# Kernel tuning notes

Hardware: AMD Instinct MI355X
Metric: run time of the kernel (lower is better)

The kernel has to match this reference:

```python
import jax, jax.numpy as jnp
import numpy as np

T_NUM = 1024      # tracks
DET_NUM = 1024    # detections
DEG = 64          # candidate detections per track
E = T_NUM * DEG   # directed track->det edges (row<col half)
N = T_NUM + DET_NUM
D_IN = 512
D_EMB = 256
LAM = 5.0
SLACK = -0.2
SINKHORN_ITERS = 8


def setup_inputs() -> dict:
    key = jax.random.key(0)
    ks = jax.random.split(key, 20)
    x = jax.random.normal(ks[0], (N, D_IN), jnp.float32)
    coords = jax.random.uniform(ks[1], (N, 4), dtype=jnp.float32)
    r = jax.random.uniform(ks[2], (N, 4), dtype=jnp.float32)
    bx1 = r[:, 0] * 100.0; by1 = r[:, 1] * 100.0
    bw = r[:, 2] * 50.0 + 1.0; bh = r[:, 3] * 50.0 + 1.0
    coords_original = jnp.stack([bx1, by1, bx1 + bw, by1 + bh], axis=1)
    src_t = jnp.repeat(jnp.arange(T_NUM, dtype=jnp.int32), DEG)
    off = jnp.tile(jnp.arange(DEG, dtype=jnp.int32), T_NUM)
    dst_d = (src_t * 13 + off) % DET_NUM            # unique det per (track, slot)
    src = src_t
    dst = dst_d + T_NUM                              # detection node ids come after tracks
    edge_index = jnp.concatenate([jnp.stack([src, dst]), jnp.stack([dst, src])], axis=1)
    ground_truth = jax.random.bernoulli(ks[3], 0.1, (T_NUM * DET_NUM,)).astype(jnp.float32)

    def lin(k, i, o):
        return jax.random.normal(k, (i, o), jnp.float32) / np.sqrt(i).astype(np.float32)

    params = {
        'W_enc': lin(ks[4], D_IN, D_EMB), 'b_enc': jnp.zeros((D_EMB,), jnp.float32),
        'W1a': lin(ks[5], 2 * D_EMB, 64), 'b1a': jnp.zeros((64,), jnp.float32),
        'W2a': lin(ks[6], 64, 1), 'b2a': jnp.zeros((1,), jnp.float32),
        'W1g': lin(ks[7], 8, 16), 'b1g': jnp.zeros((16,), jnp.float32),
        'W2g': lin(ks[8], 16, 1), 'b2g': jnp.zeros((1,), jnp.float32),
        'W1f': lin(ks[9], 2, 8), 'b1f': jnp.zeros((8,), jnp.float32),
        'W2f': lin(ks[10], 8, 1), 'b2f': jnp.zeros((1,), jnp.float32),
        'Wn': lin(ks[11], D_EMB, D_EMB), 'Wm': lin(ks[12], D_EMB, D_EMB),
        'bo': jnp.zeros((D_EMB,), jnp.float32),
        'W1c': lin(ks[13], 2, 8), 'b1c': jnp.zeros((8,), jnp.float32),
        'W2c': lin(ks[14], 8, 1), 'b2c': jnp.zeros((1,), jnp.float32),
    }
    out = {'x': x, 'coords': coords, 'coords_original': coords_original,
           'ground_truth': ground_truth, 'edge_index': edge_index}
    out.update(params)
    return out


def _box_iou(a, b):
    # a, b: [E, 4] boxes (x1, y1, x2, y2)
    lt = jnp.maximum(a[:, :2], b[:, :2])
    rb = jnp.minimum(a[:, 2:], b[:, 2:])
    wh = jnp.clip(rb - lt, 0.0)
    inter = wh[:, 0] * wh[:, 1]
    area_a = (a[:, 2] - a[:, 0]) * (a[:, 3] - a[:, 1])
    area_b = (b[:, 2] - b[:, 0]) * (b[:, 3] - b[:, 1])
    return inter / (area_a + area_b - inter + 1e-9)


def _sinkhorn(M):
    def body(M, _):
        M = M / (jnp.sum(M, axis=1, keepdims=True) + 1e-9)
        M = M / (jnp.sum(M, axis=0, keepdims=True) + 1e-9)
        return M, None
    M, _ = jax.lax.scan(body, M, None, length=SINKHORN_ITERS)
    return M


def _forward(x, coords, coords_original,
             W_enc, b_enc, W1a, b1a, W2a, b2a, W1g, b1g, W2g, b2g,
             W1f, b1f, W2f, b2f, Wn, Wm, bo, W1c, b1c, W2c, b2c,
             edge_index):
    node = jax.nn.relu(x @ W_enc + b_enc)                      # [N, D_EMB]
    src, dst = edge_index[0], edge_index[1]                    # [2E]
    # batched per-edge appearance affinity (replaces python edge loop)
    pair = jnp.concatenate([node[src], node[dst]], axis=1)     # [2E, 2*D_EMB]
    a1 = jax.nn.relu(pair @ W1a + b1a) @ W2a + b2a             # [2E, 1]
    geo = jnp.concatenate([coords[src], coords[dst]], axis=1)  # [2E, 8]
    a2 = jax.nn.relu(geo @ W1g + b1g) @ W2g + b2g              # [2E, 1]
    e_in = jnp.concatenate([a1, a2], axis=1)                   # [2E, 2]
    edge_emb = jax.nn.relu(e_in @ W1f + b1f) @ W2f + b2f       # [2E, 1]
    # optim_net: one round of edge-weighted message passing
    msg = jax.ops.segment_sum(edge_emb * node[src], dst, num_segments=N)
    out = jax.nn.relu(node @ Wn + msg @ Wm + bo)               # [N, D_EMB]
    # forward (row < col) edges are the first E entries by construction
    sf, df = src[:E], dst[:E]
    oa, ob = out[sf], out[df]
    denom = jnp.maximum(jnp.linalg.norm(oa, axis=1) * jnp.linalg.norm(ob, axis=1), 1e-6)
    cosv = jnp.sum(oa * ob, axis=1) / denom                    # CosineSimilarity(dim=0) per edge
    iou = _box_iou(coords_original[sf], coords_original[df])   # [E]
    f_in = jnp.stack([cosv, iou], axis=1)                      # [E, 2]
    aff = (jax.nn.relu(f_in @ W1c + b1c) @ W2c + b2c)[:, 0]    # [E]
    # assignment matrix with slack row/col, scatter exp(aff*lam)
    slack_val = jnp.exp(jnp.float32(SLACK * LAM))
    M = jnp.full((T_NUM + 1, DET_NUM + 1), slack_val, jnp.float32)
    M = M.at[:T_NUM, :DET_NUM].set(0.0)
    M = M.at[sf, df - T_NUM].set(jnp.exp(aff * LAM))
    M = _sinkhorn(M)
    return M[:-1, :-1].reshape(-1)                             # [T_NUM*DET_NUM]


def reference(x, coords, coords_original, ground_truth, edge_index,
              W_enc, b_enc, W1a, b1a, W2a, b2a, W1g, b1g, W2g, b2g,
              W1f, b1f, W2f, b2f, Wn, Wm, bo, W1c, b1c, W2c, b2c):
    normalized_output = _forward(x, coords, coords_original,
                                 W_enc, b_enc, W1a, b1a, W2a, b2a,
                                 W1g, b1g, W2g, b2g, W1f, b1f, W2f, b2f,
                                 Wn, Wm, bo, W1c, b1c, W2c, b2c, edge_index)
    det_num = jnp.asarray(DET_NUM, jnp.int32)
    tracklet_num = jnp.asarray(T_NUM, jnp.int32)
    return (normalized_output, ground_truth, det_num, tracklet_num)
```

## Files before the change

kernel.cpp:

```cpp
#include <hip/hip_runtime.h>

#define T_NUM 1024
#define DET_NUM 1024
#define E_NUM 65536
#define TWO_E 131072
#define N_NODES 2048
#define D_IN 512
#define D_EMB 256

__device__ __forceinline__ unsigned bf16r(float x) {
  const unsigned u = __float_as_uint(x);
  return (u + 0x7fffu + ((u >> 16) & 1u)) >> 16;
}
__device__ __forceinline__ float bflo(unsigned p) { return __uint_as_float(p << 16); }
__device__ __forceinline__ float bfhi(unsigned p) { return __uint_as_float(p & 0xffff0000u); }
__device__ __forceinline__ void fma4(float4& a, float s, const float4 w) {
  a.x = fmaf(s, w.x, a.x); a.y = fmaf(s, w.y, a.y);
  a.z = fmaf(s, w.z, a.z); a.w = fmaf(s, w.w, a.w);
}

__global__ __launch_bounds__(512) void k_enc_pg(
    const float* __restrict__ x, const float* __restrict__ W,
    const float* __restrict__ b, const float* __restrict__ coords,
    const float* __restrict__ W1a, const float* __restrict__ W1g,
    float* __restrict__ node, float* __restrict__ P1, float* __restrict__ P2,
    float* __restrict__ G1, float* __restrict__ G2) {
  __shared__ __align__(16) float xsh[4][D_IN];
  __shared__ __align__(16) float pg[8][4][D_EMB];
  __shared__ __align__(16) float ns[4][D_EMB];
  __shared__ float pp1[4][64], pp2[4][64];
  const int tid = threadIdx.x;
  const int row0 = blockIdx.x * 4;
  {
    const int idx = tid * 4;
    const int r = idx >> 9, c = idx & 511;
    *reinterpret_cast<float4*>(&xsh[r][c]) =
        *reinterpret_cast<const float4*>(x + (size_t)(row0 + r) * D_IN + c);
  }
  __syncthreads();
  {
    const int kq = __builtin_amdgcn_readfirstlane(tid >> 6);
    const int jq = tid & 63;
    const float4* W4 = (const float4*)W;
    float4 a0 = make_float4(0.f, 0.f, 0.f, 0.f);
    float4 a1 = a0, a2 = a0, a3 = a0;
    const int kbeg = kq * 64;
    for (int k = kbeg; k < kbeg + 64; ++k) {
      const float4 w4 = W4[k * 64 + jq];
      fma4(a0, xsh[0][k], w4);
      fma4(a1, xsh[1][k], w4);
      fma4(a2, xsh[2][k], w4);
      fma4(a3, xsh[3][k], w4);
    }
    *reinterpret_cast<float4*>(&pg[kq][0][4 * jq]) = a0;
    *reinterpret_cast<float4*>(&pg[kq][1][4 * jq]) = a1;
    *reinterpret_cast<float4*>(&pg[kq][2][4 * jq]) = a2;
    *reinterpret_cast<float4*>(&pg[kq][3][4 * jq]) = a3;
  }
  __syncthreads();
  {
    const int r = tid >> 7, jc = tid & 127;
    float v0 = b[2 * jc + 0], v1 = b[2 * jc + 1];
#pragma unroll
    for (int kq = 0; kq < 8; kq++) {
      v0 += pg[kq][r][2 * jc + 0];
      v1 += pg[kq][r][2 * jc + 1];
    }
    v0 = fmaxf(v0, 0.f); v1 = fmaxf(v1, 0.f);
    *reinterpret_cast<float2*>(node + (size_t)(row0 + r) * D_EMB + 2 * jc) =
        make_float2(v0, v1);
    ns[r][2 * jc] = v0; ns[r][2 * jc + 1] = v1;
  }
  __syncthreads();
  const int r2 = tid >> 7, q2 = (tid >> 6) & 1, hh = tid & 63;
  float a1 = 0.f, a2 = 0.f;
  {
    const int k0 = q2 * 128;
    for (int k = 0; k < 128; k += 4) {
      const float4 nv = *reinterpret_cast<const float4*>(&ns[r2][k0 + k]);
      a1 = fmaf(nv.x, W1a[(k0 + k + 0) * 64 + hh], a1);
      a1 = fmaf(nv.y, W1a[(k0 + k + 1) * 64 + hh], a1);
      a1 = fmaf(nv.z, W1a[(k0 + k + 2) * 64 + hh], a1);
      a1 = fmaf(nv.w, W1a[(k0 + k + 3) * 64 + hh], a1);
      a2 = fmaf(nv.x, W1a[(D_EMB + k0 + k + 0) * 64 + hh], a2);
      a2 = fmaf(nv.y, W1a[(D_EMB + k0 + k + 1) * 64 + hh], a2);
      a2 = fmaf(nv.z, W1a[(D_EMB + k0 + k + 2) * 64 + hh], a2);
      a2 = fmaf(nv.w, W1a[(D_EMB + k0 + k + 3) * 64 + hh], a2);
    }
    if (q2 == 1) { pp1[r2][hh] = a1; pp2[r2][hh] = a2; }
  }
  __syncthreads();
  if (q2 == 0) {
    P1[(size_t)(row0 + r2) * 64 + hh] = a1 + pp1[r2][hh];
    P2[(size_t)(row0 + r2) * 64 + hh] = a2 + pp2[r2][hh];
  }
  if (tid < 64) {
    const int r = tid >> 4, g = tid & 15;
    const int n = row0 + r;
    float g1 = 0.f, g2 = 0.f;
#pragma unroll
    for (int k = 0; k < 4; k++) {
      const float c = coords[(size_t)n * 4 + k];
      g1 = fmaf(c, W1g[k * 16 + g], g1);
      g2 = fmaf(c, W1g[(4 + k) * 16 + g], g2);
    }
    G1[(size_t)n * 16 + g] = g1;
    G2[(size_t)n * 16 + g] = g2;
  }
}

__global__ __launch_bounds__(512) void k_msg_out(
    const float* __restrict__ node,
    const float* __restrict__ P1, const float* __restrict__ P2,
    const float* __restrict__ G1, const float* __restrict__ G2,
    const float* __restrict__ b1a, const float* __restrict__ W2a, const float* __restrict__ b2a,
    const float* __restrict__ b1g, const float* __restrict__ W2g, const float* __restrict__ b2g,
    const float* __restrict__ W1f, const float* __restrict__ b1f,
    const float* __restrict__ W2f, const float* __restrict__ b2f,
    const float* __restrict__ Wn, const float* __restrict__ Wm,
    const float* __restrict__ bo, float* __restrict__ outE, float* __restrict__ nrm) {
  __shared__ __align__(16) float msp[2][4][D_EMB];
  __shared__ __align__(16) float ms[4][D_EMB];
  __shared__ __align__(16) float nsh[4][D_EMB];
  __shared__ __align__(16) float pg[8][4][D_EMB];
  __shared__ float wsh[4][64];
  __shared__ int ssh[4][64];
  __shared__ float pa1[4][64], pa2[4][64];
  __shared__ float redn[8];
  const int tid = threadIdx.x;
  const int h = __builtin_amdgcn_readfirstlane(tid >> 8);
  const int j = tid & 255;
  const int row0 = blockIdx.x * 4;
  {
    const int r = (tid >> 6) & 3, o = tid & 63;
    const int n = row0 + r;
    int src;
    if (n < T_NUM) {
      src = T_NUM + ((13 * n + o) & 1023);
    } else {
      const int d = n - T_NUM;
      src = (709 * (d - o)) & 1023;
    }
    float a1p = 0.f, a2p = 0.f;
    const float4* p1 = (const float4*)(P1 + (size_t)src * 64) + h * 8;
    const float4* p2 = (const float4*)(P2 + (size_t)n * 64) + h * 8;
    const float4* b1 = (const float4*)b1a + h * 8;
    const float4* w2 = (const float4*)W2a + h * 8;
#pragma unroll
    for (int i = 0; i < 8; i++) {
      const float4 pa = p1[i], pb = p2[i], bb = b1[i], ww = w2[i];
      a1p += fmaxf(pa.x + pb.x + bb.x, 0.f) * ww.x + fmaxf(pa.y + pb.y + bb.y, 0.f) * ww.y +
             fmaxf(pa.z + pb.z + bb.z, 0.f) * ww.z + fmaxf(pa.w + pb.w + bb.w, 0.f) * ww.w;
    }
    const float4* g1 = (const float4*)(G1 + (size_t)src * 16) + h * 2;
    const float4* g2 = (const float4*)(G2 + (size_t)n * 16) + h * 2;
    const float4* bg = (const float4*)b1g + h * 2;
    const float4* wg = (const float4*)W2g + h * 2;
#pragma unroll
    for (int i = 0; i < 2; i++) {
      const float4 pa = g1[i], pb = g2[i], bb = bg[i], ww = wg[i];
      a2p += fmaxf(pa.x + pb.x + bb.x, 0.f) * ww.x + fmaxf(pa.y + pb.y + bb.y, 0.f) * ww.y +
             fmaxf(pa.z + pb.z + bb.z, 0.f) * ww.z + fmaxf(pa.w + pb.w + bb.w, 0.f) * ww.w;
    }
    if (h == 1) { pa1[r][o] = a1p; pa2[r][o] = a2p; ssh[r][o] = src; }
    else        { wsh[r][o] = a1p; pg[0][r][o] = a2p; }
  }
  __syncthreads();
  if (h == 0) {
    const int r = (tid >> 6) & 3, o = tid & 63;
    const float a1 = wsh[r][o] + pa1[r][o] + b2a[0];
    const float a2 = pg[0][r][o] + pa2[r][o] + b2g[0];
    float acc = b2f[0];
#pragma unroll
    for (int jj = 0; jj < 8; jj++) {
      const float hv = fmaxf(a1 * W1f[jj] + a2 * W1f[8 + jj] + b1f[jj], 0.f);
      acc = fmaf(hv, W2f[jj], acc);
    }
    wsh[r][o] = acc;
  } else {
#pragma unroll
    for (int rr = 0; rr < 4; rr++)
      nsh[rr][j] = node[(size_t)(row0 + rr) * D_EMB + j];
  }
  __syncthreads();
  {
    const int s = tid >> 8;
    const int r = (tid >> 6) & 3;
    const int qd = tid & 63;
    const int i0 = s * 32;
    float ax = 0.f, ay = 0.f, az = 0.f, aw = 0.f;
#pragma unroll 4
    for (int i = 0; i < 32; i++) {
      const float w = wsh[r][i0 + i];
      const float4 nv = *reinterpret_cast<const float4*>(
          node + (size_t)ssh[r][i0 + i] * D_EMB + 4 * qd);
      ax = fmaf(w, nv.x, ax); ay = fmaf(w, nv.y, ay);
      az = fmaf(w, nv.z, az); aw = fmaf(w, nv.w, aw);
    }
    *reinterpret_cast<float4*>(&msp[s][r][4 * qd]) = make_float4(ax, ay, az, aw);
  }
  __syncthreads();
  {
    float* m0 = &ms[0][0];
    const float* s0 = &msp[0][0][0];
    const float* s1 = &msp[1][0][0];
    m0[tid] = s0[tid] + s1[tid];
    m0[tid + 512] = s0[tid + 512] + s1[tid + 512];
  }
  __syncthreads();
  {
    const int kq = __builtin_amdgcn_readfirstlane(tid >> 6);
    const int jq = tid & 63;
    const float4* Wn4 = (const float4*)Wn;
    const float4* Wm4 = (const float4*)Wm;
    float4 a0 = make_float4(0.f, 0.f, 0.f, 0.f);
    float4 a1 = a0, a2 = a0, a3 = a0;
    const int kbeg = kq * 32;
    for (int k = kbeg; k < kbeg + 32; ++k) {
      const float4 wn = Wn4[k * 64 + jq];
      const float4 wm = Wm4[k * 64 + jq];
      const float n0 = nsh[0][k], m0v = ms[0][k];
      const float n1 = nsh[1][k], m1v = ms[1][k];
      const float n2 = nsh[2][k], m2v = ms[2][k];
      const float n3 = nsh[3][k], m3v = ms[3][k];
      fma4(a0, n0, wn); fma4(a0, m0v, wm);
      fma4(a1, n1, wn); fma4(a1, m1v, wm);
      fma4(a2, n2, wn); fma4(a2, m2v, wm);
      fma4(a3, n3, wn); fma4(a3, m3v, wm);
    }
    *reinterpret_cast<float4*>(&pg[kq][0][4 * jq]) = a0;
    *reinterpret_cast<float4*>(&pg[kq][1][4 * jq]) = a1;
    *reinterpret_cast<float4*>(&pg[kq][2][4 * jq]) = a2;
    *reinterpret_cast<float4*>(&pg[kq][3][4 * jq]) = a3;
  }
  __syncthreads();
  {
    const int r = tid >> 7, jc = tid & 127;
    const int lane = tid & 63, wid = tid >> 6;
    float v0 = bo[2 * jc + 0], v1 = bo[2 * jc + 1];
#pragma unroll
    for (int kq = 0; kq < 8; kq++) {
      v0 += pg[kq][r][2 * jc + 0];
      v1 += pg[kq][r][2 * jc + 1];
    }
    v0 = fmaxf(v0, 0.f); v1 = fmaxf(v1, 0.f);
    *reinterpret_cast<float2*>(outE + (size_t)(row0 + r) * D_EMB + 2 * jc) =
        make_float2(v0, v1);
    float sq = v0 * v0 + v1 * v1;
#pragma unroll
    for (int oo = 32; oo > 0; oo >>= 1) sq += __shfl_down(sq, oo, 64);
    if (lane == 0) redn[wid] = sq;
  }
  __syncthreads();
  if (tid < 4)
    nrm[row0 + tid] = sqrtf(redn[2 * tid] + redn[2 * tid + 1]);
}

__global__ __launch_bounds__(256) void k_aff(
    const float* __restrict__ outE, const float* __restrict__ nrm,
    const float* __restrict__ cov,
    const float* __restrict__ W1c, const float* __restrict__ b1c,
    const float* __restrict__ W2c, const float* __restrict__ b2c,
    float* __restrict__ Kbp, unsigned short* __restrict__ KTg) {
  __shared__ __align__(16) float4 oas[64];
  __shared__ float psum[4][64];
  const int t = blockIdx.x;
  const int tid = threadIdx.x;
  const int o = tid & 63, c = tid >> 6;
  const int s = t;
  if (tid < 64) oas[tid] = ((const float4*)(outE + (size_t)s * D_EMB))[tid];
  __syncthreads();
  const int d = (13 * t + o) & 1023;
  const int dn = T_NUM + d;
  {
    const float4* ob = (const float4*)(outE + (size_t)dn * D_EMB) + c * 16;
    const float4* oa = oas + c * 16;
    float dot = 0.f;
#pragma unroll
    for (int i = 0; i < 16; i++) {
      const float4 a = oa[i], bq = ob[i];
      dot += a.x * bq.x + a.y * bq.y + a.z * bq.z + a.w * bq.w;
    }
    psum[c][o] = dot;
  }
  __syncthreads();
  if (tid < 64) {
    const float dot = psum[0][o] + psum[1][o] + psum[2][o] + psum[3][o];
    const float cosv = dot / fmaxf(nrm[s] * nrm[dn], 1e-6f);
    const float4 A = ((const float4*)cov)[s];
    const float4 B = ((const float4*)cov)[dn];
    const float ltx = fmaxf(A.x, B.x), lty = fmaxf(A.y, B.y);
    const float rbx = fminf(A.z, B.z), rby = fminf(A.w, B.w);
    const float wx = fmaxf(rbx - ltx, 0.f), wy = fmaxf(rby - lty, 0.f);
    const float inter = wx * wy;
    const float areaA = (A.z - A.x) * (A.w - A.y);
    const float areaB = (B.z - B.x) * (B.w - B.y);
    const float iou = inter / (areaA + areaB - inter + 1e-9f);
    float aff = b2c[0];
#pragma unroll
    for (int jj = 0; jj < 8; jj++) {
      const float h = fmaxf(cosv * W1c[jj] + iou * W1c[8 + jj] + b1c[jj], 0.f);
      aff = fmaf(h, W2c[jj], aff);
    }
    const float Kv = __expf(aff * 5.0f);
    const int tp = (13 * s) & 1023;
    Kbp[tp * 68 + (tp & 3) + o] = Kv;
    if (o < 4) {
      const int pr = (o < (tp & 3)) ? o : o + 64;
      Kbp[tp * 68 + pr] = 0.f;
    }
    const int cbase = (((d & 1022) + 960) & 1023) & ~3;
    const int rho = (((d + 961) & 1023) - cbase) & 1023;
    KTg[d * 72 + rho + 63 - o] = (unsigned short)bf16r(Kv);
    if (o < 8) {
      const int slot = (o < rho) ? o : o + 64;
      KTg[d * 72 + slot] = 0;
    }
  }
}

__global__ __launch_bounds__(512, 2) void k_sinkhorn(
    const float* __restrict__ Kbp, const unsigned short* __restrict__ KTg,
    float* __restrict__ ug, float* __restrict__ vg,
    const float* __restrict__ gt, float* __restrict__ out) {
  if (blockIdx.x != 0) {
    const size_t idx = (size_t)(blockIdx.x - 1) * 512 + threadIdx.x;
    ((float4*)out)[(size_t)T_NUM * 256 + idx] = ((const float4*)gt)[idx];
    return;
  }
  __shared__ __align__(16) float u_lds[1092];
  __shared__ __align__(16) float v_lds[1092];
  __shared__ float red_u[8];
  __shared__ float red_v[8];
  __shared__ __align__(16) uint4 ktlA[9][512];
  __shared__ __align__(16) uint4 ktlB[9][512];
  const int tid = threadIdx.x;
  const int lane = tid & 63, wid = tid >> 6;
  const int ra = 2 * tid, rb = 2 * tid + 1;
  const int qa = (ra & ~3) >> 2;
  const int cbase = ((ra + 960) & 1023) & ~3;
  const int qc = cbase >> 2;
  unsigned k0[34], k1[34];
  {
    const float4* s0p = (const float4*)(Kbp + (size_t)ra * 68);
    const float4* s1p = (const float4*)(Kbp + (size_t)rb * 68);
#pragma unroll
    for (int c = 0; c < 17; c++) {
      float4 f = s0p[c];
      k0[2 * c]     = bf16r(f.x) | (bf16r(f.y) << 16);
      k0[2 * c + 1] = bf16r(f.z) | (bf16r(f.w) << 16);
      f = s1p[c];
      k1[2 * c]     = bf16r(f.x) | (bf16r(f.y) << 16);
      k1[2 * c + 1] = bf16r(f.z) | (bf16r(f.w) << 16);
    }
  }
  {
    const uint4* g = (const uint4*)KTg;
#pragma unroll
    for (int q = 0; q < 9; q++) ktlA[q][tid] = g[tid * 18 + q];
#pragma unroll
    for (int q = 0; q < 9; q++) ktlB[q][tid] = g[tid * 18 + 9 + q];
  }
  float u0 = 1.f, u1 = 1.f, vc0 = 1.f, vc1 = 1.f, u_sl = 1.f, v_sl = 1.f;
  v_lds[tid] = 1.f; v_lds[tid + 512] = 1.f;
  if (tid < 68) v_lds[1024 + tid] = 1.f;
  if (tid < 8) red_v[tid] = 128.f;
  const float slack = 0.36787944117144233f;
  __syncthreads();
#pragma unroll 1
  for (int it = 0; it < 8; ++it) {
    const float4* vq = (const float4*)v_lds;
    float a00 = 0.f, a01 = 0.f, a10 = 0.f, a11 = 0.f;
#pragma unroll
    for (int c = 0; c < 17; c++) {
      const float4 v4 = vq[qa + c];
      unsigned p = k0[2 * c];
      a00 = fmaf(bflo(p), v4.x, a00); a00 = fmaf(bfhi(p), v4.y, a00);
      p = k0[2 * c + 1];
      a01 = fmaf(bflo(p), v4.z, a01); a01 = fmaf(bfhi(p), v4.w, a01);
      p = k1[2 * c];
      a10 = fmaf(bflo(p), v4.x, a10); a10 = fmaf(bfhi(p), v4.y, a10);
      p = k1[2 * c + 1];
      a11 = fmaf(bflo(p), v4.z, a11); a11 = fmaf(bfhi(p), v4.w, a11);
    }
    const float sumv = red_v[0] + red_v[1] + red_v[2] + red_v[3] +
                       red_v[4] + red_v[5] + red_v[6] + red_v[7];
    const float s0 = a00 + a01 + slack * v_sl;
    const float s1 = a10 + a11 + slack * v_sl;
    u0 = u0 / (u0 * s0 + 1e-9f);
    u1 = u1 / (u1 * s1 + 1e-9f);
    u_sl = u_sl / (u_sl * slack * (sumv + v_sl) + 1e-9f);
    u_lds[ra] = u0; u_lds[rb] = u1;
    if (tid < 34) { u_lds[1024 + ra] = u0; u_lds[1024 + rb] = u1; }
    float usum = u0 + u1;
#pragma unroll
    for (int o = 32; o > 0; o >>= 1) usum += __shfl_down(usum, o, 64);
    if (lane == 0) red_u[wid] = usum;
    __syncthreads();
    const float4* uq = (const float4*)u_lds;
    float t0 = 0.f, t1 = 0.f;
#pragma unroll 3
    for (int q = 0; q < 9; q++) {
      const uint4 A = ktlA[q][tid];
      const uint4 B = ktlB[q][tid];
      const float4 ua = uq[qc + 2 * q];
      const float4 ub = uq[qc + 2 * q + 1];
      t0 = fmaf(bflo(A.x), ua.x, t0); t0 = fmaf(bfhi(A.x), ua.y, t0);
      t0 = fmaf(bflo(A.y), ua.z, t0); t0 = fmaf(bfhi(A.y), ua.w, t0);
      t0 = fmaf(bflo(A.z), ub.x, t0); t0 = fmaf(bfhi(A.z), ub.y, t0);
      t0 = fmaf(bflo(A.w), ub.z, t0); t0 = fmaf(bfhi(A.w), ub.w, t0);
      t1 = fmaf(bflo(B.x), ua.x, t1); t1 = fmaf(bfhi(B.x), ua.y, t1);
      t1 = fmaf(bflo(B.y), ua.z, t1); t1 = fmaf(bfhi(B.y), ua.w, t1);
      t1 = fmaf(bflo(B.z), ub.x, t1); t1 = fmaf(bfhi(B.z), ub.y, t1);
      t1 = fmaf(bflo(B.w), ub.z, t1); t1 = fmaf(bfhi(B.w), ub.w, t1);
    }
    const float sumu = red_u[0] + red_u[1] + red_u[2] + red_u[3] +
                       red_u[4] + red_u[5] + red_u[6] + red_u[7];
    t0 += slack * u_sl;
    t1 += slack * u_sl;
    vc0 = vc0 / (vc0 * t0 + 1e-9f);
    vc1 = vc1 / (vc1 * t1 + 1e-9f);
    v_sl = v_sl / (v_sl * slack * (sumu + u_sl) + 1e-9f);
    v_lds[ra] = vc0; v_lds[rb] = vc1;
    if (tid < 34) { v_lds[1024 + ra] = vc0; v_lds[1024 + rb] = vc1; }
    float vsum = vc0 + vc1;
#pragma unroll
    for (int o = 32; o > 0; o >>= 1) vsum += __shfl_down(vsum, o, 64);
    if (lane == 0) red_v[wid] = vsum;
    __syncthreads();
  }
  ((float2*)ug)[tid] = make_float2(u0, u1);
  ((float2*)vg)[tid] = make_float2(vc0, vc1);
}

__global__ __launch_bounds__(256) void k_final(
    const float* __restrict__ Kbp, const float* __restrict__ ug,
    const float* __restrict__ vg, float* __restrict__ out) {
  const int t = blockIdx.x;
  const int tp = (13 * t) & 1023;
  const float u = ug[tp];
  const float* krow = Kbp + (size_t)tp * 68 + (tp & 3);
  const int d0 = threadIdx.x * 4;
  const float4 v4 = ((const float4*)vg)[threadIdx.x];
  float4 o4;
  const int m0 = (d0 - tp) & 1023;
  const int m1 = (d0 + 1 - tp) & 1023;
  const int m2 = (d0 + 2 - tp) & 1023;
  const int m3 = (d0 + 3 - tp) & 1023;
  o4.x = (m0 < 64) ? u * krow[m0] * v4.x : 0.f;
  o4.y = (m1 < 64) ? u * krow[m1] * v4.y : 0.f;
  o4.z = (m2 < 64) ? u * krow[m2] * v4.z : 0.f;
  o4.w = (m3 < 64) ? u * krow[m3] * v4.w : 0.f;
  ((float4*)out)[(size_t)t * 256 + threadIdx.x] = o4;
  if (t == 0 && threadIdx.x == 0) {
    out[(size_t)2 * T_NUM * DET_NUM] = 1024.0f;
    out[(size_t)2 * T_NUM * DET_NUM + 1] = 1024.0f;
  }
}

extern "C" void kernel_launch(void* const* d_in, const int* in_sizes, int n_in,
                              void* d_out, int out_size, void* d_ws, size_t ws_size,
                              hipStream_t stream) {
  const float* x      = (const float*)d_in[0];
  const float* coords = (const float*)d_in[1];
  const float* cov    = (const float*)d_in[2];
  const float* gt     = (const float*)d_in[3];
  const float* W_enc  = (const float*)d_in[5];
  const float* b_enc  = (const float*)d_in[6];
  const float* W1a    = (const float*)d_in[7];
  const float* b1a    = (const float*)d_in[8];
  const float* W2a    = (const float*)d_in[9];
  const float* b2a    = (const float*)d_in[10];
  const float* W1g    = (const float*)d_in[11];
  const float* b1g    = (const float*)d_in[12];
  const float* W2g    = (const float*)d_in[13];
  const float* b2g    = (const float*)d_in[14];
  const float* W1f    = (const float*)d_in[15];
  const float* b1f    = (const float*)d_in[16];
  const float* W2f    = (const float*)d_in[17];
  const float* b2f    = (const float*)d_in[18];
  const float* Wn     = (const float*)d_in[19];
  const float* Wm     = (const float*)d_in[20];
  const float* bo     = (const float*)d_in[21];
  const float* W1c    = (const float*)d_in[22];
  const float* b1c    = (const float*)d_in[23];
  const float* W2c    = (const float*)d_in[24];
  const float* b2c    = (const float*)d_in[25];

  char* ws = (char*)d_ws;
  size_t off = 0;
  auto alloc = [&](size_t bytes) {
    char* p = ws + off;
    off = (off + bytes + 255) & ~(size_t)255;
    return p;
  };
  float* node  = (float*)alloc((size_t)N_NODES * D_EMB * 4);
  float* P1    = (float*)alloc((size_t)N_NODES * 64 * 4);
  float* P2    = (float*)alloc((size_t)N_NODES * 64 * 4);
  float* G1    = (float*)alloc((size_t)N_NODES * 16 * 4);
  float* G2    = (float*)alloc((size_t)N_NODES * 16 * 4);
  float* outE  = (float*)alloc((size_t)N_NODES * D_EMB * 4);
  float* nrm   = (float*)alloc((size_t)N_NODES * 4);
  float* Kbp   = (float*)alloc((size_t)1024 * 68 * 4);
  unsigned short* KTg = (unsigned short*)alloc((size_t)1024 * 72 * 2);
  float* ug    = (float*)alloc(1024 * 4);
  float* vg    = (float*)alloc(1024 * 4);
  float* out   = (float*)d_out;

  k_enc_pg<<<N_NODES / 4, 512, 0, stream>>>(x, W_enc, b_enc, coords, W1a, W1g,
                                            node, P1, P2, G1, G2);
  k_msg_out<<<N_NODES / 4, 512, 0, stream>>>(node, P1, P2, G1, G2,
                                             b1a, W2a, b2a, b1g, W2g, b2g,
                                             W1f, b1f, W2f, b2f,
                                             Wn, Wm, bo, outE, nrm);
  k_aff<<<T_NUM, 256, 0, stream>>>(outE, nrm, cov, W1c, b1c, W2c, b2c,
                                   Kbp, KTg);
  k_sinkhorn<<<513, 512, 0, stream>>>(Kbp, KTg, ug, vg, gt, out);
  k_final<<<T_NUM, 256, 0, stream>>>(Kbp, ug, vg, out);
}
```

Measured before the change: 193.8 us.

## Run Sinkhorn with one row per thread using 1024-thread block

The single-block Sinkhorn kernel now uses 1024 threads, with each thread owning one row and one column instead of two of each. This halves the serial dependent FMA chain per thread in both the row and column passes. The cost is twice the waves per barrier and reductions over 16 wave partials instead of 8. The ground-truth copy blocks are resized to match the larger block.

```diff
diff --git a/kernel.cpp b/kernel.cpp
--- a/kernel.cpp
+++ b/kernel.cpp
@@ -319,118 +319,98 @@
   }
 }
 
-__global__ __launch_bounds__(512, 2) void k_sinkhorn(
+__global__ __launch_bounds__(1024) void k_sinkhorn(
     const float* __restrict__ Kbp, const unsigned short* __restrict__ KTg,
     float* __restrict__ ug, float* __restrict__ vg,
     const float* __restrict__ gt, float* __restrict__ out) {
   if (blockIdx.x != 0) {
-    const size_t idx = (size_t)(blockIdx.x - 1) * 512 + threadIdx.x;
+    const size_t idx = (size_t)(blockIdx.x - 1) * 1024 + threadIdx.x;
     ((float4*)out)[(size_t)T_NUM * 256 + idx] = ((const float4*)gt)[idx];
     return;
   }
   __shared__ __align__(16) float u_lds[1092];
   __shared__ __align__(16) float v_lds[1092];
-  __shared__ float red_u[8];
-  __shared__ float red_v[8];
-  __shared__ __align__(16) uint4 ktlA[9][512];
-  __shared__ __align__(16) uint4 ktlB[9][512];
+  __shared__ float red_u[16];
+  __shared__ float red_v[16];
+  __shared__ __align__(16) uint4 ktl[9][1024];
   const int tid = threadIdx.x;
   const int lane = tid & 63, wid = tid >> 6;
-  const int ra = 2 * tid, rb = 2 * tid + 1;
-  const int qa = (ra & ~3) >> 2;
-  const int cbase = ((ra + 960) & 1023) & ~3;
-  const int qc = cbase >> 2;
-  unsigned k0[34], k1[34];
-  {
-    const float4* s0p = (const float4*)(Kbp + (size_t)ra * 68);
-    const float4* s1p = (const float4*)(Kbp + (size_t)rb * 68);
+  unsigned kr[34];
+  {
+    const float4* sp = (const float4*)(Kbp + (size_t)tid * 68);
 #pragma unroll
     for (int c = 0; c < 17; c++) {
-      float4 f = s0p[c];
-      k0[2 * c]     = bf16r(f.x) | (bf16r(f.y) << 16);
-      k0[2 * c + 1] = bf16r(f.z) | (bf16r(f.w) << 16);
-      f = s1p[c];
-      k1[2 * c]     = bf16r(f.x) | (bf16r(f.y) << 16);
-      k1[2 * c + 1] = bf16r(f.z) | (bf16r(f.w) << 16);
+      const float4 f = sp[c];
+      kr[2 * c]     = bf16r(f.x) | (bf16r(f.y) << 16);
+      kr[2 * c + 1] = bf16r(f.z) | (bf16r(f.w) << 16);
     }
   }
   {
     const uint4* g = (const uint4*)KTg;
 #pragma unroll
-    for (int q = 0; q < 9; q++) ktlA[q][tid] = g[tid * 18 + q];
-#pragma unroll
-    for (int q = 0; q < 9; q++) ktlB[q][tid] = g[tid * 18 + 9 + q];
-  }
-  float u0 = 1.f, u1 = 1.f, vc0 = 1.f, vc1 = 1.f, u_sl = 1.f, v_sl = 1.f;
-  v_lds[tid] = 1.f; v_lds[tid + 512] = 1.f;
+    for (int q = 0; q < 9; q++) ktl[q][tid] = g[tid * 9 + q];
+  }
+  const int qa = tid & ~3;
+  const int cb = (((tid & ~1) + 960) & 1023) & ~3;
+  float u = 1.f, v = 1.f, u_sl = 1.f, v_sl = 1.f;
+  v_lds[tid] = 1.f;
   if (tid < 68) v_lds[1024 + tid] = 1.f;
-  if (tid < 8) red_v[tid] = 128.f;
+  if (tid < 16) red_v[tid] = 64.f;
   const float slack = 0.36787944117144233f;
   __syncthreads();
 #pragma unroll 1
   for (int it = 0; it < 8; ++it) {
-    const float4* vq = (const float4*)v_lds;
-    float a00 = 0.f, a01 = 0.f, a10 = 0.f, a11 = 0.f;
+    const float4* vq = (const float4*)(v_lds + qa);
+    float a0 = 0.f, a1 = 0.f;
 #pragma unroll
     for (int c = 0; c < 17; c++) {
-      const float4 v4 = vq[qa + c];
-      unsigned p = k0[2 * c];
-      a00 = fmaf(bflo(p), v4.x, a00); a00 = fmaf(bfhi(p), v4.y, a00);
-      p = k0[2 * c + 1];
-      a01 = fmaf(bflo(p), v4.z, a01); a01 = fmaf(bfhi(p), v4.w, a01);
-      p = k1[2 * c];
-      a10 = fmaf(bflo(p), v4.x, a10); a10 = fmaf(bfhi(p), v4.y, a10);
-      p = k1[2 * c + 1];
-      a11 = fmaf(bflo(p), v4.z, a11); a11 = fmaf(bfhi(p), v4.w, a11);
-    }
-    const float sumv = red_v[0] + red_v[1] + red_v[2] + red_v[3] +
-                       red_v[4] + red_v[5] + red_v[6] + red_v[7];
-    const float s0 = a00 + a01 + slack * v_sl;
-    const float s1 = a10 + a11 + slack * v_sl;
-    u0 = u0 / (u0 * s0 + 1e-9f);
-    u1 = u1 / (u1 * s1 + 1e-9f);
+      const float4 v4 = vq[c];
+      unsigned p = kr[2 * c];
+      a0 = fmaf(bflo(p), v4.x, a0); a0 = fmaf(bfhi(p), v4.y, a0);
+      p = kr[2 * c + 1];
+      a1 = fmaf(bflo(p), v4.z, a1); a1 = fmaf(bfhi(p), v4.w, a1);
+    }
+    float sumv = 0.f;
+#pragma unroll
+    for (int i = 0; i < 16; i++) sumv += red_v[i];
+    const float s = a0 + a1 + slack * v_sl;
+    u = u / (u * s + 1e-9f);
     u_sl = u_sl / (u_sl * slack * (sumv + v_sl) + 1e-9f);
-    u_lds[ra] = u0; u_lds[rb] = u1;
-    if (tid < 34) { u_lds[1024 + ra] = u0; u_lds[1024 + rb] = u1; }
-    float usum = u0 + u1;
+    u_lds[tid] = u;
+    if (tid < 68) u_lds[1024 + tid] = u;
+    float usum = u;
 #pragma unroll
     for (int o = 32; o > 0; o >>= 1) usum += __shfl_down(usum, o, 64);
     if (lane == 0) red_u[wid] = usum;
     __syncthreads();
-    const float4* uq = (const float4*)u_lds;
+    const float4* uq = (const float4*)(u_lds + cb);
     float t0 = 0.f, t1 = 0.f;
 #pragma unroll 3
     for (int q = 0; q < 9; q++) {
-      const uint4 A = ktlA[q][tid];
-      const uint4 B = ktlB[q][tid];
-      const float4 ua = uq[qc + 2 * q];
-      const float4 ub = uq[qc + 2 * q + 1];
+      const uint4 A = ktl[q][tid];
+      const float4 ua = uq[2 * q];
+      const float4 ub = uq[2 * q + 1];
       t0 = fmaf(bflo(A.x), ua.x, t0); t0 = fmaf(bfhi(A.x), ua.y, t0);
       t0 = fmaf(bflo(A.y), ua.z, t0); t0 = fmaf(bfhi(A.y), ua.w, t0);
-      t0 = fmaf(bflo(A.z), ub.x, t0); t0 = fmaf(bfhi(A.z), ub.y, t0);
-      t0 = fmaf(bflo(A.w), ub.z, t0); t0 = fmaf(bfhi(A.w), ub.w, t0);
-      t1 = fmaf(bflo(B.x), ua.x, t1); t1 = fmaf(bfhi(B.x), ua.y, t1);
-      t1 = fmaf(bflo(B.y), ua.z, t1); t1 = fmaf(bfhi(B.y), ua.w, t1);
-      t1 = fmaf(bflo(B.z), ub.x, t1); t1 = fmaf(bfhi(B.z), ub.y, t1);
-      t1 = fmaf(bflo(B.w), ub.z, t1); t1 = fmaf(bfhi(B.w), ub.w, t1);
-    }
-    const float sumu = red_u[0] + red_u[1] + red_u[2] + red_u[3] +
-                       red_u[4] + red_u[5] + red_u[6] + red_u[7];
-    t0 += slack * u_sl;
-    t1 += slack * u_sl;
-    vc0 = vc0 / (vc0 * t0 + 1e-9f);
-    vc1 = vc1 / (vc1 * t1 + 1e-9f);
+      t1 = fmaf(bflo(A.z), ub.x, t1); t1 = fmaf(bfhi(A.z), ub.y, t1);
+      t1 = fmaf(bflo(A.w), ub.z, t1); t1 = fmaf(bfhi(A.w), ub.w, t1);
+    }
+    float sumu = 0.f;
+#pragma unroll
+    for (int i = 0; i < 16; i++) sumu += red_u[i];
+    const float tv = t0 + t1 + slack * u_sl;
+    v = v / (v * tv + 1e-9f);
     v_sl = v_sl / (v_sl * slack * (sumu + u_sl) + 1e-9f);
-    v_lds[ra] = vc0; v_lds[rb] = vc1;
-    if (tid < 34) { v_lds[1024 + ra] = vc0; v_lds[1024 + rb] = vc1; }
-    float vsum = vc0 + vc1;
+    v_lds[tid] = v;
+    if (tid < 68) v_lds[1024 + tid] = v;
+    float vsum = v;
 #pragma unroll
     for (int o = 32; o > 0; o >>= 1) vsum += __shfl_down(vsum, o, 64);
     if (lane == 0) red_v[wid] = vsum;
     __syncthreads();
   }
-  ((float2*)ug)[tid] = make_float2(u0, u1);
-  ((float2*)vg)[tid] = make_float2(vc0, vc1);
+  ug[tid] = u;
+  vg[tid] = v;
 }
 
 __global__ __launch_bounds__(256) void k_final(
@@ -515,6 +495,6 @@
                                              Wn, Wm, bo, outE, nrm);
   k_aff<<<T_NUM, 256, 0, stream>>>(outE, nrm, cov, W1c, b1c, W2c, b2c,
                                    Kbp, KTg);
-  k_sinkhorn<<<513, 512, 0, stream>>>(Kbp, KTg, ug, vg, gt, out);
+  k_sinkhorn<<<257, 1024, 0, stream>>>(Kbp, KTg, ug, vg, gt, out);
   k_final<<<T_NUM, 256, 0, stream>>>(Kbp, ug, vg, out);
 }
```

Result: slower. 198.8 us (+2.6%).
